# Kernel tuning notes

Measured on AMD Instinct MI355X. Metric: run time of the kernel, lower is better.

The kernel has to match this reference:

```python
import jax, jax.numpy as jnp
import numpy as np

B, S, D = 4, 2048, 768
LN_EPS = 1e-12


def setup_inputs() -> dict:
    key = jax.random.key(0)
    k0, k1, k2, k3 = jax.random.split(key, 4)
    scale = 1.0 / np.sqrt(D).astype(np.float32)
    return {
        "hidden_states": jax.random.normal(k0, (B, S, D), jnp.float32),
        "attention_mask": jnp.ones((B, 1, S, S), jnp.int32),
        "prior_n_attn": jax.random.uniform(k1, (B, S, S), jnp.float32),
        "ln_w": jnp.ones((D,), jnp.float32),
        "ln_b": jnp.zeros((D,), jnp.float32),
        "wq": jax.random.normal(k2, (D, D), jnp.float32) * scale,
        "bq": jnp.zeros((D,), jnp.float32),
        "wk": jax.random.normal(k3, (D, D), jnp.float32) * scale,
        "bk": jnp.zeros((D,), jnp.float32),
    }


def reference(hidden_states, attention_mask, prior_n_attn, ln_w, ln_b, wq, bq, wk, bk):
    _, S_, D_ = hidden_states.shape
    # LayerNorm (biased variance, as torch.nn.LayerNorm)
    mu = hidden_states.mean(-1, keepdims=True)
    var = ((hidden_states - mu) ** 2).mean(-1, keepdims=True)
    h = (hidden_states - mu) / jnp.sqrt(var + LN_EPS) * ln_w + ln_b

    a = jnp.eye(S_, k=1, dtype=jnp.int32)      # superdiagonal
    bI = jnp.eye(S_, dtype=jnp.int32)          # diagonal
    c = jnp.eye(S_, k=-1, dtype=jnp.int32)     # subdiagonal
    tri = jnp.triu(jnp.ones((S_, S_), jnp.float32))

    # mask & (a + c): band of width 1 off the diagonal; then squeeze dim 1
    mask = (attention_mask.astype(jnp.int32) & (a + c))[:, 0]  # [B,S,S]

    q = h @ wq + bq
    k = h @ wk + bk
    scores = jnp.einsum("bsd,btd->bst", q, k) / D_
    scores = jnp.where(mask == 0, -jnp.inf, scores)
    n = jnp.nan_to_num(jax.nn.softmax(scores, axis=-1))
    n = jnp.sqrt(n * jnp.swapaxes(n, -2, -1) + 1e-9)
    n = prior_n_attn + (1.0 - prior_n_attn) * n

    # keep only the superdiagonal of log(n + 1e-9); zero elsewhere
    logm = jnp.log(n + 1e-9) * a.astype(n.dtype)
    # prefix-sum via triangular matmuls (same math as torch source)
    t = logm @ tri                                   # [B,S,S]
    g = jnp.exp(jnp.einsum("ij,bjk->bik", tri, t))   # [B,S,S]
    su = tri - bI.astype(tri.dtype)                  # strictly-upper indicator
    g = g * su                                       # masked_fill((tri-b)==0, 0)
    diag_part = jnp.where(bI == 0, 1e-9, n)          # n.masked_fill(b==0, 1e-9)
    g = g + jnp.swapaxes(g, -2, -1) + diag_part
    return (g, n)
```

## Files before the change

### kernel.cpp

```cpp
#include <hip/hip_runtime.h>
#include <hip/hip_bf16.h>
#include <math.h>
#include <stdint.h>

#define BB 4
#define SS 2048
#define DD 768
#define MM (BB*SS)

typedef __attribute__((ext_vector_type(4))) float  f32x4;
typedef __attribute__((ext_vector_type(8))) __bf16 bf16x8;
typedef __attribute__((ext_vector_type(4))) __bf16 bf16x4;

#define AS1 __attribute__((address_space(1)))
#define AS3 __attribute__((address_space(3)))

__global__ __launch_bounds__(256) void combined_kernel(
        const float* __restrict__ x, const float* __restrict__ lw,
        const float* __restrict__ lb, const float* __restrict__ wq,
        const float* __restrict__ wk, const float* __restrict__ bq,
        const float* __restrict__ bk, const int* __restrict__ att,
        const float* __restrict__ prior, __bf16* __restrict__ G,
        float* __restrict__ u, float* __restrict__ v, float* __restrict__ cb,
        __bf16* __restrict__ h, int* __restrict__ fl, float* __restrict__ prsup) {
    __shared__ __attribute__((aligned(16))) __bf16 As[64][32];
    __shared__ __attribute__((aligned(16))) __bf16 Bs[64][32];
    const int bid = blockIdx.x;
    if (bid >= 2577) {
        const int idx = (bid - 2577) * 256 + threadIdx.x;
        const int b = idx >> 11, s = idx & 2047;
        const bool au = (s < SS - 1) && ((att[((size_t)b * SS + s) * SS + (s + 1)] & 1) != 0);
        const bool ad = (s > 0)      && ((att[((size_t)b * SS + s) * SS + (s - 1)] & 1) != 0);
        fl[idx] = (au ? 1 : 0) | (ad ? 2 : 0);
        if (s < SS - 1)
            prsup[idx] = prior[((size_t)b * SS + s) * SS + s + 1];
        return;
    }
    if (bid >= 529) {
        const int row = (bid - 529) * 4 + (threadIdx.x >> 6);
        const int lane = threadIdx.x & 63;
        const float* xr = x + (size_t)row * DD + lane * 12;
        f32x4 a0 = *(const f32x4*)(xr), a1 = *(const f32x4*)(xr + 4), a2 = *(const f32x4*)(xr + 8);
        float xs[12];
#pragma unroll
        for (int c = 0; c < 4; c++) { xs[c] = a0[c]; xs[4 + c] = a1[c]; xs[8 + c] = a2[c]; }
        float s = 0.f, ss = 0.f;
#pragma unroll
        for (int c = 0; c < 12; c++) { s += xs[c]; ss += xs[c] * xs[c]; }
#pragma unroll
        for (int o = 1; o < 64; o <<= 1) { s += __shfl_xor(s, o); ss += __shfl_xor(ss, o); }
        const float mu = s * (1.0f / DD);
        const float var = ss * (1.0f / DD) - mu * mu;
        const float rstd = 1.0f / sqrtf(var + 1e-12f);
        const float* wp = lw + lane * 12; const float* bp = lb + lane * 12;
        f32x4 w0 = *(const f32x4*)(wp), w1 = *(const f32x4*)(wp + 4), w2 = *(const f32x4*)(wp + 8);
        f32x4 b0 = *(const f32x4*)(bp), b1 = *(const f32x4*)(bp + 4), b2 = *(const f32x4*)(bp + 8);
        bf16x4 o0, o1, o2;
#pragma unroll
        for (int c = 0; c < 4; c++) {
            o0[c] = (__bf16)((xs[c]     - mu) * rstd * w0[c] + b0[c]);
            o1[c] = (__bf16)((xs[4 + c] - mu) * rstd * w1[c] + b1[c]);
            o2[c] = (__bf16)((xs[8 + c] - mu) * rstd * w2[c] + b2[c]);
        }
        __bf16* hr = h + (size_t)row * DD + lane * 12;
        *(bf16x4*)(hr) = o0; *(bf16x4*)(hr + 4) = o1; *(bf16x4*)(hr + 8) = o2;
        return;
    }
    if (bid >= 144) {
        const int id = bid - 144;
        const int lane = threadIdx.x & 63, wv_ = threadIdx.x >> 6;
        if (id == 384) {
            if (wv_ != 0) return;
            float s = 0.f;
#pragma unroll
            for (int m = 0; m < 12; m++) s += bq[lane + 64 * m] * bk[lane + 64 * m];
#pragma unroll
            for (int o = 1; o < 64; o <<= 1) s += __shfl_xor(s, o);
            if (lane == 0) cb[0] = s;
            return;
        }
        const bool isU = id < 192;
        const int row = (isU ? id : id - 192) * 4 + wv_;
        const float* W = isU ? wq : wk;
        const float* bvec = isU ? bk : bq;
        const float* wr_ = W + (size_t)row * DD;
        float s = 0.f;
#pragma unroll
        for (int m = 0; m < 12; m++) s += wr_[lane + 64 * m] * bvec[lane + 64 * m];
#pragma unroll
        for (int o = 1; o < 64; o <<= 1) s += __shfl_xor(s, o);
        if (lane == 0) (isU ? u : v)[row] = s;
        return;
    }
    const int m0 = (bid % 12) * 64;
    const int n0 = (bid / 12) * 64;
    const int t = threadIdx.x;
    const int wave = t >> 6, lane = t & 63;
    const int wr = wave >> 1, wc = wave & 1;
    const int srow = t >> 2, scol = (t & 3) * 8;
    f32x4 acc[2][2] = {};

    for (int k0 = 0; k0 < DD; k0 += 32) {
        const float* ga = wq + (size_t)(m0 + srow) * DD + k0 + scol;
        const float* gb = wk + (size_t)(n0 + srow) * DD + k0 + scol;
        f32x4 a0 = *(const f32x4*)(ga), a1 = *(const f32x4*)(ga + 4);
        f32x4 b0 = *(const f32x4*)(gb), b1 = *(const f32x4*)(gb + 4);
        bf16x8 av, bv;
#pragma unroll
        for (int c = 0; c < 4; c++) {
            av[c] = (__bf16)a0[c]; av[4 + c] = (__bf16)a1[c];
            bv[c] = (__bf16)b0[c]; bv[4 + c] = (__bf16)b1[c];
        }
        __syncthreads();
        *(bf16x8*)&As[srow][scol] = av;
        *(bf16x8*)&Bs[srow][scol] = bv;
        __syncthreads();
        const int r = lane & 15, ko = (lane >> 4) << 3;
        bf16x8 af[2], bvf[2];
#pragma unroll
        for (int i = 0; i < 2; i++) af[i]  = *(const bf16x8*)&As[wr * 32 + i * 16 + r][ko];
#pragma unroll
        for (int j = 0; j < 2; j++) bvf[j] = *(const bf16x8*)&Bs[wc * 32 + j * 16 + r][ko];
#pragma unroll
        for (int i = 0; i < 2; i++)
#pragma unroll
            for (int j = 0; j < 2; j++)
                acc[i][j] = __builtin_amdgcn_mfma_f32_16x16x32_bf16(af[i], bvf[j], acc[i][j], 0, 0, 0);
    }
#pragma unroll
    for (int i = 0; i < 2; i++) {
        const int mm = m0 + wr * 32 + i * 16 + (lane >> 4) * 4;
#pragma unroll
        for (int j = 0; j < 2; j++) {
            const int nn = n0 + wc * 32 + j * 16 + (lane & 15);
#pragma unroll
            for (int rr = 0; rr < 4; rr++)
                G[(size_t)(mm + rr) * DD + nn] = (__bf16)acc[i][j][rr];
        }
    }
}

__global__ __launch_bounds__(256) void rgemm_kernel(const __bf16* __restrict__ A,
        const __bf16* __restrict__ Bt, const float* __restrict__ u,
        const float* __restrict__ v, float* __restrict__ du_part,
        float* __restrict__ dn_part, float* __restrict__ w_part) {
    __shared__ __attribute__((aligned(16))) __bf16 As[64][32];
    __shared__ __attribute__((aligned(16))) __bf16 Bs[128][32];
    const int bid = blockIdx.x;
    const int mt = bid & 127, nt = bid >> 7;
    const int m0 = mt * 64, n0 = nt * 128;
    const int t = threadIdx.x;
    const int wave = t >> 6, lane = t & 63;
    const int wr = wave >> 1, wc = wave & 1;
    f32x4 acc[2][4] = {};

    char* asb = (char*)&As[0][0];
    char* bsb = (char*)&Bs[0][0];
    const int rA = (wave << 4) + (lane >> 2);
    const int cA = (lane & 3) << 3;

    for (int k0 = 0; k0 < DD; k0 += 32) {
        const __bf16* ga  = A  + (size_t)(m0 + rA) * DD + k0 + cA;
        const __bf16* gb0 = Bt + (size_t)(n0 + rA) * DD + k0 + cA;
        const __bf16* gb1 = gb0 + (size_t)64 * DD;
        __builtin_amdgcn_global_load_lds((const AS1 void*)(ga),  (AS3 void*)(asb + wave * 1024),        16, 0, 0);
        __builtin_amdgcn_global_load_lds((const AS1 void*)(gb0), (AS3 void*)(bsb + wave * 1024),        16, 0, 0);
        __builtin_amdgcn_global_load_lds((const AS1 void*)(gb1), (AS3 void*)(bsb + 4096 + wave * 1024), 16, 0, 0);
        __syncthreads();
        const int r = lane & 15, ko = (lane >> 4) << 3;
        bf16x8 af[2], bvf[4];
#pragma unroll
        for (int i = 0; i < 2; i++) af[i]  = *(const bf16x8*)&As[wr * 32 + i * 16 + r][ko];
#pragma unroll
        for (int j = 0; j < 4; j++) bvf[j] = *(const bf16x8*)&Bs[wc * 64 + j * 16 + r][ko];
#pragma unroll
        for (int i = 0; i < 2; i++)
#pragma unroll
            for (int j = 0; j < 4; j++)
                acc[i][j] = __builtin_amdgcn_mfma_f32_16x16x32_bf16(af[i], bvf[j], acc[i][j], 0, 0, 0);
        __syncthreads();
    }
    int colg[4]; float ub[4], vb[4];
#pragma unroll
    for (int j = 0; j < 4; j++) {
        colg[j] = n0 + wc * 64 + j * 16 + (lane & 15);
        ub[j] = u[colg[j]];
        vb[j] = v[colg[j]];
    }
    const int slot = nt * 2 + wc;
#pragma unroll
    for (int i = 0; i < 2; i++) {
#pragma unroll
        for (int rr = 0; rr < 4; rr++) {
            const int row = m0 + wr * 32 + i * 16 + (lane >> 4) * 4 + rr;
            const int rm = (row == 0) ? 0 : row - 1;
            const int rp = (row == MM - 1) ? MM - 1 : row + 1;
            const __bf16* hm = A + (size_t)rm * DD;
            const __bf16* hz = A + (size_t)row * DD;
            const __bf16* hp = A + (size_t)rp * DD;
            float dua = 0.f, dna = 0.f, wa = 0.f;
#pragma unroll
            for (int j = 0; j < 4; j++) {
                const float Rv = acc[i][j][rr] + ub[j];
                dua += Rv * (float)hm[colg[j]];
                dna += Rv * (float)hp[colg[j]];
                wa  += vb[j] * (float)hz[colg[j]];
            }
#pragma unroll
            for (int o = 1; o < 16; o <<= 1) {
                dua += __shfl_xor(dua, o);
                dna += __shfl_xor(dna, o);
                wa  += __shfl_xor(wa, o);
            }
            if ((lane & 15) == 0) {
                du_part[slot * MM + row] = dua;
                dn_part[slot * MM + row] = dna;
                w_part [slot * MM + row] = wa;
            }
        }
    }
}

__global__ __launch_bounds__(256) void scan_kernel(const float* __restrict__ du_part,
        const float* __restrict__ dn_part, const float* __restrict__ w_part,
        const float* __restrict__ cbp, const int* __restrict__ fl_i,
        const float* __restrict__ prsup,
        float* __restrict__ nb, double* __restrict__ P2) {
    const int b = blockIdx.x;
    const int t = threadIdx.x;
    __shared__ float du_s[SS], dn_s[SS], w_s[SS], sh_pd[SS];
    __shared__ double warr[256];
    for (int x = t; x < SS; x += 256) {
        const int idx = b * SS + x;
        float d1 = 0.f, d2 = 0.f, d3 = 0.f;
#pragma unroll
        for (int p = 0; p < 12; p++) {
            d1 += du_part[p * MM + idx];
            d2 += dn_part[p * MM + idx];
            d3 += w_part [p * MM + idx];
        }
        du_s[x] = d1; dn_s[x] = d2; w_s[x] = d3;
    }
    __syncthreads();
    const float cb = cbp[0];
    float pu_r[8];
#pragma unroll
    for (int e = 0; e < 8; e++) {
        const int s = t * 8 + e;
        const int fl = fl_i[b * SS + s];
        const bool au = fl & 1, ad = fl & 2;
        float puv = 0.f, pdv = 0.f;
        if (au || ad) {
            const float eu = au ? (du_s[s + 1] + w_s[s + 1] + cb) * (1.0f / DD) : 0.f;
            const float ed = ad ? (dn_s[s - 1] + w_s[s - 1] + cb) * (1.0f / DD) : 0.f;
            float mx = au ? eu : ed;
            if (au && ad) mx = fmaxf(eu, ed);
            const float zu = au ? expf(eu - mx) : 0.f;
            const float zd = ad ? expf(ed - mx) : 0.f;
            const float iz = 1.f / (zu + zd);
            puv = zu * iz; pdv = zd * iz;
        }
        pu_r[e] = puv;
        sh_pd[s] = pdv;
    }
    __syncthreads();
    double L[8];
    double mysum = 0.0;
#pragma unroll
    for (int e = 0; e < 8; e++) {
        const int s = t * 8 + e;
        double Lv = 0.0;
        float nbv = 0.f;
        if (s < SS - 1) {
            nbv = sqrtf(pu_r[e] * sh_pd[s + 1] + 1e-9f);
            const float pr = prsup[b * SS + s];
            const float nsup = pr + (1.f - pr) * nbv;
            Lv = (double)log2f(nsup + 1e-9f);
        }
        nb[b * SS + s] = nbv;
        L[e] = Lv; mysum += Lv;
    }
    warr[t] = mysum;
    __syncthreads();
    for (int o = 1; o < 256; o <<= 1) {
        double vv = 0.0;
        if (t >= o) vv = warr[t - o];
        __syncthreads();
        if (t >= o) warr[t] += vv;
        __syncthreads();
    }
    double run = warr[t] - mysum;
#pragma unroll
    for (int e = 0; e < 8; e++) {
        P2[(size_t)b * SS + t * 8 + e] = run;
        run += L[e];
    }
}

__global__ __launch_bounds__(256) void out_kernel(const float* __restrict__ prior,
        const float* __restrict__ nb, const double* __restrict__ P2,
        float* __restrict__ gout, float* __restrict__ nout) {
    const size_t t8 = (size_t)blockIdx.x * 256 + threadIdx.x;
    const int b = (int)(t8 >> 19);
    const size_t off = t8 << 3;
    const size_t r = off & ((1u << 22) - 1);
    const int i  = (int)(r >> 11);
    const int k0 = (int)(r & 2047);
    const f32x4 p0 = *(const f32x4*)(prior + off);
    const f32x4 p1 = *(const f32x4*)(prior + off + 4);
    const double* Pb = P2 + ((size_t)b << 11);
    const double Pi = Pb[i];
    const float* nbb = nb + ((size_t)b << 11);
    f32x4 g0, g1, n0, n1;
#pragma unroll
    for (int c = 0; c < 8; c++) {
        const int k = k0 + c;
        const float pr = (c < 4) ? p0[c] : p1[c - 4];
        float vv = 3.16227766016838e-5f;
        if (k == i + 1)      vv = nbb[i];
        else if (k == i - 1) vv = nbb[k];
        const float nval = pr + (1.f - pr) * vv;
        float g;
        if (k == i) {
            g = nval;
        } else {
            const double Pk = Pb[k];
            const double dd = (k > i) ? (Pk - Pi) : (Pi - Pk);
            g = exp2f((float)dd) + 1e-9f;
        }
        if (c < 4) { g0[c] = g; n0[c] = nval; }
        else       { g1[c - 4] = g; n1[c - 4] = nval; }
    }
    *(f32x4*)(gout + off)     = g0;
    *(f32x4*)(gout + off + 4) = g1;
    *(f32x4*)(nout + off)     = n0;
    *(f32x4*)(nout + off + 4) = n1;
}

extern "C" void kernel_launch(void* const* d_in, const int* in_sizes, int n_in,
                              void* d_out, int out_size, void* d_ws, size_t ws_size,
                              hipStream_t stream) {
    const float* hs    = (const float*)d_in[0];
    const int*   att   = (const int*)d_in[1];
    const float* prior = (const float*)d_in[2];
    const float* ln_w  = (const float*)d_in[3];
    const float* ln_b  = (const float*)d_in[4];
    const float* wq    = (const float*)d_in[5];
    const float* bq    = (const float*)d_in[6];
    const float* wk    = (const float*)d_in[7];
    const float* bk    = (const float*)d_in[8];

    float* gout = (float*)d_out;
    float* nout = gout + (size_t)BB * SS * SS;

    char* ws = (char*)d_ws;
    __bf16* h       = (__bf16*)(ws);
    __bf16* G       = (__bf16*)(ws + 12582912);
    float*  u       = (float*) (ws + 13762560);
    float*  v       = (float*) (ws + 13765632);
    float*  cbp     = (float*) (ws + 13768704);
    int*    fl      = (int*)   (ws + 13768960);
    float*  prsup   = (float*) (ws + 13801728);
    float*  du_part = (float*) (ws + 13834496);
    float*  dn_part = (float*) (ws + 14227712);
    float*  w_part  = (float*) (ws + 14620928);
    float*  nbuf    = (float*) (ws + 15014144);
    double* P2      = (double*)(ws + 15046912);

    combined_kernel<<<dim3(2609), dim3(256), 0, stream>>>(hs, ln_w, ln_b, wq, wk, bq, bk,
                                                          att, prior, G, u, v, cbp, h, fl, prsup);
    rgemm_kernel<<<dim3(768), dim3(256), 0, stream>>>(h, G, u, v, du_part, dn_part, w_part);
    scan_kernel<<<dim3(BB), dim3(256), 0, stream>>>(du_part, dn_part, w_part, cbp, fl, prsup, nbuf, P2);
    out_kernel<<<dim3((BB * SS * SS / 8) / 256), dim3(256), 0, stream>>>(prior, nbuf, P2, gout, nout);
}
```

Before: 100.4 us.

## Deepen rgemm K-tile with swizzled LDS, atomic partial reduction, nontemporal output I/O

The rgemm kernel now stages 64-wide K tiles, halving the loop trips and barriers. Its LDS layout uses an XOR swizzle to avoid bank conflicts on the fragment reads. The 12-slot partial-sum buffers are replaced by float atomicAdd into zeroed accumulators, which cuts the scan kernel's reduction reads but makes the summation order nondeterministic. The out kernel also switches to nontemporal loads and stores for the large streaming prior and output arrays, to reduce cache pollution.

```diff
diff --git a/kernel.cpp b/kernel.cpp
--- a/kernel.cpp
+++ b/kernel.cpp
@@ -22,7 +22,8 @@
         const float* __restrict__ bk, const int* __restrict__ att,
         const float* __restrict__ prior, __bf16* __restrict__ G,
         float* __restrict__ u, float* __restrict__ v, float* __restrict__ cb,
-        __bf16* __restrict__ h, int* __restrict__ fl, float* __restrict__ prsup) {
+        __bf16* __restrict__ h, int* __restrict__ fl, float* __restrict__ prsup,
+        float* __restrict__ du_g, float* __restrict__ dn_g, float* __restrict__ w_g) {
     __shared__ __attribute__((aligned(16))) __bf16 As[64][32];
     __shared__ __attribute__((aligned(16))) __bf16 Bs[64][32];
     const int bid = blockIdx.x;
@@ -34,6 +35,7 @@
         fl[idx] = (au ? 1 : 0) | (ad ? 2 : 0);
         if (s < SS - 1)
             prsup[idx] = prior[((size_t)b * SS + s) * SS + s + 1];
+        du_g[idx] = 0.f; dn_g[idx] = 0.f; w_g[idx] = 0.f;
         return;
     }
     if (bid >= 529) {
@@ -142,10 +144,10 @@
 
 __global__ __launch_bounds__(256) void rgemm_kernel(const __bf16* __restrict__ A,
         const __bf16* __restrict__ Bt, const float* __restrict__ u,
-        const float* __restrict__ v, float* __restrict__ du_part,
-        float* __restrict__ dn_part, float* __restrict__ w_part) {
-    __shared__ __attribute__((aligned(16))) __bf16 As[64][32];
-    __shared__ __attribute__((aligned(16))) __bf16 Bs[128][32];
+        const float* __restrict__ v, float* __restrict__ du_g,
+        float* __restrict__ dn_g, float* __restrict__ w_g) {
+    __shared__ __attribute__((aligned(16))) __bf16 As[64 * 64];
+    __shared__ __attribute__((aligned(16))) __bf16 Bs[128 * 64];
     const int bid = blockIdx.x;
     const int mt = bid & 127, nt = bid >> 7;
     const int m0 = mt * 64, n0 = nt * 128;
@@ -154,30 +156,51 @@
     const int wr = wave >> 1, wc = wave & 1;
     f32x4 acc[2][4] = {};
 
-    char* asb = (char*)&As[0][0];
-    char* bsb = (char*)&Bs[0][0];
-    const int rA = (wave << 4) + (lane >> 2);
-    const int cA = (lane & 3) << 3;
-
-    for (int k0 = 0; k0 < DD; k0 += 32) {
-        const __bf16* ga  = A  + (size_t)(m0 + rA) * DD + k0 + cA;
-        const __bf16* gb0 = Bt + (size_t)(n0 + rA) * DD + k0 + cA;
-        const __bf16* gb1 = gb0 + (size_t)64 * DD;
-        __builtin_amdgcn_global_load_lds((const AS1 void*)(ga),  (AS3 void*)(asb + wave * 1024),        16, 0, 0);
-        __builtin_amdgcn_global_load_lds((const AS1 void*)(gb0), (AS3 void*)(bsb + wave * 1024),        16, 0, 0);
-        __builtin_amdgcn_global_load_lds((const AS1 void*)(gb1), (AS3 void*)(bsb + 4096 + wave * 1024), 16, 0, 0);
-        __syncthreads();
-        const int r = lane & 15, ko = (lane >> 4) << 3;
-        bf16x8 af[2], bvf[4];
-#pragma unroll
-        for (int i = 0; i < 2; i++) af[i]  = *(const bf16x8*)&As[wr * 32 + i * 16 + r][ko];
-#pragma unroll
-        for (int j = 0; j < 4; j++) bvf[j] = *(const bf16x8*)&Bs[wc * 64 + j * 16 + r][ko];
-#pragma unroll
-        for (int i = 0; i < 2; i++)
-#pragma unroll
-            for (int j = 0; j < 4; j++)
-                acc[i][j] = __builtin_amdgcn_mfma_f32_16x16x32_bf16(af[i], bvf[j], acc[i][j], 0, 0, 0);
+    char* asb = (char*)As;
+    char* bsb = (char*)Bs;
+    const int lrow = lane >> 3;
+    const int slot = lane & 7;
+
+    for (int k0 = 0; k0 < DD; k0 += 64) {
+#pragma unroll
+        for (int i = 0; i < 2; i++) {
+            const int j = wave * 2 + i;
+            const int row = j * 8 + lrow;
+            const int scol = (slot ^ (row & 7)) << 3;
+            const __bf16* ga = A + (size_t)(m0 + row) * DD + k0 + scol;
+            __builtin_amdgcn_global_load_lds((const AS1 void*)ga, (AS3 void*)(asb + j * 1024), 16, 0, 0);
+        }
+#pragma unroll
+        for (int i = 0; i < 4; i++) {
+            const int j = wave * 4 + i;
+            const int row = j * 8 + lrow;
+            const int scol = (slot ^ (row & 7)) << 3;
+            const __bf16* gb = Bt + (size_t)(n0 + row) * DD + k0 + scol;
+            __builtin_amdgcn_global_load_lds((const AS1 void*)gb, (AS3 void*)(bsb + j * 1024), 16, 0, 0);
+        }
+        __syncthreads();
+        const int r = lane & 15;
+        const int cbase = (lane >> 4) << 3;
+#pragma unroll
+        for (int kk = 0; kk < 2; kk++) {
+            const int C = cbase + kk * 32;
+            bf16x8 af[2], bvf[4];
+#pragma unroll
+            for (int i = 0; i < 2; i++) {
+                const int R = wr * 32 + i * 16 + r;
+                af[i] = *(const bf16x8*)&As[R * 64 + (C ^ ((R & 7) << 3))];
+            }
+#pragma unroll
+            for (int j = 0; j < 4; j++) {
+                const int R = wc * 64 + j * 16 + r;
+                bvf[j] = *(const bf16x8*)&Bs[R * 64 + (C ^ ((R & 7) << 3))];
+            }
+#pragma unroll
+            for (int i = 0; i < 2; i++)
+#pragma unroll
+                for (int j = 0; j < 4; j++)
+                    acc[i][j] = __builtin_amdgcn_mfma_f32_16x16x32_bf16(af[i], bvf[j], acc[i][j], 0, 0, 0);
+        }
         __syncthreads();
     }
     int colg[4]; float ub[4], vb[4];
@@ -187,7 +210,6 @@
         ub[j] = u[colg[j]];
         vb[j] = v[colg[j]];
     }
-    const int slot = nt * 2 + wc;
 #pragma unroll
     for (int i = 0; i < 2; i++) {
 #pragma unroll
@@ -213,16 +235,16 @@
                 wa  += __shfl_xor(wa, o);
             }
             if ((lane & 15) == 0) {
-                du_part[slot * MM + row] = dua;
-                dn_part[slot * MM + row] = dna;
-                w_part [slot * MM + row] = wa;
-            }
-        }
-    }
-}
-
-__global__ __launch_bounds__(256) void scan_kernel(const float* __restrict__ du_part,
-        const float* __restrict__ dn_part, const float* __restrict__ w_part,
+                atomicAdd(&du_g[row], dua);
+                atomicAdd(&dn_g[row], dna);
+                atomicAdd(&w_g[row], wa);
+            }
+        }
+    }
+}
+
+__global__ __launch_bounds__(256) void scan_kernel(const float* __restrict__ du_g,
+        const float* __restrict__ dn_g, const float* __restrict__ w_g,
         const float* __restrict__ cbp, const int* __restrict__ fl_i,
         const float* __restrict__ prsup,
         float* __restrict__ nb, double* __restrict__ P2) {
@@ -231,15 +253,9 @@
     __shared__ float du_s[SS], dn_s[SS], w_s[SS], sh_pd[SS];
     __shared__ double warr[256];
     for (int x = t; x < SS; x += 256) {
-        const int idx = b * SS + x;
-        float d1 = 0.f, d2 = 0.f, d3 = 0.f;
-#pragma unroll
-        for (int p = 0; p < 12; p++) {
-            d1 += du_part[p * MM + idx];
-            d2 += dn_part[p * MM + idx];
-            d3 += w_part [p * MM + idx];
-        }
-        du_s[x] = d1; dn_s[x] = d2; w_s[x] = d3;
+        du_s[x] = du_g[b * SS + x];
+        dn_s[x] = dn_g[b * SS + x];
+        w_s[x]  = w_g[b * SS + x];
     }
     __syncthreads();
     const float cb = cbp[0];
@@ -306,8 +322,8 @@
     const size_t r = off & ((1u << 22) - 1);
     const int i  = (int)(r >> 11);
     const int k0 = (int)(r & 2047);
-    const f32x4 p0 = *(const f32x4*)(prior + off);
-    const f32x4 p1 = *(const f32x4*)(prior + off + 4);
+    const f32x4 p0 = __builtin_nontemporal_load((const f32x4*)(prior + off));
+    const f32x4 p1 = __builtin_nontemporal_load((const f32x4*)(prior + off + 4));
     const double* Pb = P2 + ((size_t)b << 11);
     const double Pi = Pb[i];
     const float* nbb = nb + ((size_t)b << 11);
@@ -331,10 +347,10 @@
         if (c < 4) { g0[c] = g; n0[c] = nval; }
         else       { g1[c - 4] = g; n1[c - 4] = nval; }
     }
-    *(f32x4*)(gout + off)     = g0;
-    *(f32x4*)(gout + off + 4) = g1;
-    *(f32x4*)(nout + off)     = n0;
-    *(f32x4*)(nout + off + 4) = n1;
+    __builtin_nontemporal_store(g0, (f32x4*)(gout + off));
+    __builtin_nontemporal_store(g1, (f32x4*)(gout + off + 4));
+    __builtin_nontemporal_store(n0, (f32x4*)(nout + off));
+    __builtin_nontemporal_store(n1, (f32x4*)(nout + off + 4));
 }
 
 extern "C" void kernel_launch(void* const* d_in, const int* in_sizes, int n_in,
@@ -354,22 +370,23 @@
     float* nout = gout + (size_t)BB * SS * SS;
 
     char* ws = (char*)d_ws;
-    __bf16* h       = (__bf16*)(ws);
-    __bf16* G       = (__bf16*)(ws + 12582912);
-    float*  u       = (float*) (ws + 13762560);
-    float*  v       = (float*) (ws + 13765632);
-    float*  cbp     = (float*) (ws + 13768704);
-    int*    fl      = (int*)   (ws + 13768960);
-    float*  prsup   = (float*) (ws + 13801728);
-    float*  du_part = (float*) (ws + 13834496);
-    float*  dn_part = (float*) (ws + 14227712);
-    float*  w_part  = (float*) (ws + 14620928);
-    float*  nbuf    = (float*) (ws + 15014144);
-    double* P2      = (double*)(ws + 15046912);
+    __bf16* h     = (__bf16*)(ws);
+    __bf16* G     = (__bf16*)(ws + 12582912);
+    float*  u     = (float*) (ws + 13762560);
+    float*  v     = (float*) (ws + 13765632);
+    float*  cbp   = (float*) (ws + 13768704);
+    int*    fl    = (int*)   (ws + 13768960);
+    float*  prsup = (float*) (ws + 13801728);
+    float*  du_g  = (float*) (ws + 13834496);
+    float*  dn_g  = (float*) (ws + 13867264);
+    float*  w_g   = (float*) (ws + 13900032);
+    float*  nbuf  = (float*) (ws + 13932800);
+    double* P2    = (double*)(ws + 13965568);
 
     combined_kernel<<<dim3(2609), dim3(256), 0, stream>>>(hs, ln_w, ln_b, wq, wk, bq, bk,
-                                                          att, prior, G, u, v, cbp, h, fl, prsup);
-    rgemm_kernel<<<dim3(768), dim3(256), 0, stream>>>(h, G, u, v, du_part, dn_part, w_part);
-    scan_kernel<<<dim3(BB), dim3(256), 0, stream>>>(du_part, dn_part, w_part, cbp, fl, prsup, nbuf, P2);
+                                                          att, prior, G, u, v, cbp, h, fl, prsup,
+                                                          du_g, dn_g, w_g);
+    rgemm_kernel<<<dim3(768), dim3(256), 0, stream>>>(h, G, u, v, du_g, dn_g, w_g);
+    scan_kernel<<<dim3(BB), dim3(256), 0, stream>>>(du_g, dn_g, w_g, cbp, fl, prsup, nbuf, P2);
     out_kernel<<<dim3((BB * SS * SS / 8) / 256), dim3(256), 0, stream>>>(prior, nbuf, P2, gout, nout);
 }
```

Measured after the change: 105.7 us. 1.05x slower.
